# Performance work log

Measured on AMD Instinct MI355X. Metric: run time of the kernel, lower is better.

The kernel has to match this reference:

```python
import jax, jax.numpy as jnp
import numpy as np

NUM_GRAPHS = 256


def _gcn_norm(edge_index, num_nodes):
    # Add self-loops (PyG GCNConv default) and compute symmetric normalization
    loops = jnp.arange(num_nodes, dtype=edge_index.dtype)
    src = jnp.concatenate([edge_index[0], loops])
    dst = jnp.concatenate([edge_index[1], loops])
    deg = jax.ops.segment_sum(jnp.ones_like(dst, dtype=jnp.float32), dst,
                              num_segments=num_nodes)
    dinv = jnp.where(deg > 0, jax.lax.rsqrt(deg), 0.0)
    norm = dinv[src] * dinv[dst]  # [E + N]
    return src, dst, norm


def _gcn_layer(x, W, b, src, dst, norm, num_nodes):
    h = x @ W                      # transform first (cheaper: N x d_out)
    msg = h[src] * norm[:, None]   # gather + per-edge scale  [E+N, d_out]
    agg = jax.ops.segment_sum(msg, dst, num_segments=num_nodes)
    return agg + b


def setup_inputs() -> dict:
    key = jax.random.key(0)
    ks = jax.random.split(key, 12)
    N, E, F_in = 100000, 1600000, 5
    x = jax.random.normal(ks[0], (N, F_in), dtype=jnp.float32)
    edge_index = jax.random.randint(ks[1], (2, E), 0, N, dtype=jnp.int64)
    batch = jnp.sort(jax.random.randint(ks[2], (N,), 0, NUM_GRAPHS, dtype=jnp.int64))

    def glorot(k, fi, fo):
        s = jnp.sqrt(6.0 / (fi + fo))
        return jax.random.uniform(k, (fi, fo), jnp.float32, -s, s)

    return {
        "x": x, "edge_index": edge_index, "batch": batch,
        "W1": glorot(ks[3], F_in, 64), "b1": jnp.zeros((64,), jnp.float32),
        "W2": glorot(ks[4], 64, 128),  "b2": jnp.zeros((128,), jnp.float32),
        "W3": glorot(ks[5], 128, 64),  "b3": jnp.zeros((64,), jnp.float32),
        "Wfc": glorot(ks[6], 64, 1),   "bfc": jnp.zeros((1,), jnp.float32),
    }


def reference(x, edge_index, batch, W1, b1, W2, b2, W3, b3, Wfc, bfc):
    N = x.shape[0]
    src, dst, norm = _gcn_norm(edge_index, N)
    h = jax.nn.relu(_gcn_layer(x, W1, b1, src, dst, norm, N))
    h = jax.nn.relu(_gcn_layer(h, W2, b2, src, dst, norm, N))
    h = jax.nn.relu(_gcn_layer(h, W3, b3, src, dst, norm, N))
    # global mean pool over graph ids
    sums = jax.ops.segment_sum(h, batch, num_segments=NUM_GRAPHS)
    cnts = jax.ops.segment_sum(jnp.ones((N,), jnp.float32), batch,
                               num_segments=NUM_GRAPHS)
    pooled = sums / jnp.maximum(cnts, 1.0)[:, None]   # [G, 64]
    return jax.nn.sigmoid(pooled @ Wfc + bfc)         # [G, 1]
```

## Files before the change

kernel.cpp:

```cpp
#include <hip/hip_runtime.h>
#include <math.h>

#define NG 256
#define NBK 512
#define BCAP 3584
#define FBN 96

static __device__ __forceinline__ int bucket_lo(int p, int n) {
    return (int)(((long long)p * n + NBK - 1) / NBK);
}

static __device__ __forceinline__ float blo(unsigned u) {
    return __uint_as_float(u << 16);
}
static __device__ __forceinline__ float bhi(unsigned u) {
    return __uint_as_float(u & 0xFFFF0000u);
}
static __device__ __forceinline__ unsigned packbf(float a, float b) {
    unsigned ua = __float_as_uint(a);
    ua = (ua + 0x7FFFu + ((ua >> 16) & 1u)) >> 16;
    unsigned ub = __float_as_uint(b);
    ub = (ub + 0x7FFFu + ((ub >> 16) & 1u)) & 0xFFFF0000u;
    return ua | ub;
}

__global__ void zero_bcur(int* bcur) {
    int i = blockIdx.x * blockDim.x + threadIdx.x;
    if (i < NBK) bcur[i] = i * BCAP;
}

__global__ void bucketA(const int* __restrict__ src, const int* __restrict__ dst,
                        int* bcur, unsigned* stage, int e, int n) {
    __shared__ int cnt[NBK];
    __shared__ int base[NBK];
    int nb = gridDim.x;
    int c0 = (int)((long long)blockIdx.x * e / nb);
    int c1 = (int)((long long)(blockIdx.x + 1) * e / nb);
    for (int k = threadIdx.x; k < NBK; k += blockDim.x) cnt[k] = 0;
    __syncthreads();
    for (int i = c0 + threadIdx.x; i < c1; i += blockDim.x) {
        int d = dst[i];
        int p = (int)((long long)d * NBK / n);
        atomicAdd(&cnt[p], 1);
    }
    __syncthreads();
    for (int k = threadIdx.x; k < NBK; k += blockDim.x)
        base[k] = atomicAdd(&bcur[k], cnt[k]);
    __syncthreads();
    for (int k = threadIdx.x; k < NBK; k += blockDim.x) cnt[k] = 0;
    __syncthreads();
    for (int i = c0 + threadIdx.x; i < c1; i += blockDim.x) {
        int s = src[i], d = dst[i];
        int p = (int)((long long)d * NBK / n);
        int ldst = d - bucket_lo(p, n);
        int lp = atomicAdd(&cnt[p], 1);
        stage[base[p] + lp] = ((unsigned)s << 8) | (unsigned)ldst;
    }
}

__global__ void fillB2(const unsigned* __restrict__ stage,
                       const int* __restrict__ bcur,
                       int* __restrict__ rowptr, float* __restrict__ dinv,
                       int* __restrict__ csrs,
                       const float* __restrict__ x, float* __restrict__ xs,
                       int n, int e) {
    __shared__ int ldeg[256];
    __shared__ int loff[256];
    __shared__ int bstart;
    int p = blockIdx.x;
    int t = threadIdx.x;
    int lo = bucket_lo(p, n), hi = bucket_lo(p + 1, n);
    int nloc = hi - lo;

    {
        int acc = 0;
        for (int k = t; k < p; k += 256) acc += bcur[k] - k * BCAP;
        ldeg[t] = acc;
        __syncthreads();
        for (int off = 128; off > 0; off >>= 1) {
            if (t < off) ldeg[t] += ldeg[t + off];
            __syncthreads();
        }
        if (t == 0) bstart = ldeg[0];
        __syncthreads();
    }

    if (t < 256) ldeg[t] = 0;
    __syncthreads();
    int s0 = p * BCAP, s1 = bcur[p];
    for (int i = s0 + t; i < s1; i += 256)
        atomicAdd(&ldeg[stage[i] & 255u], 1);
    __syncthreads();

    int v = (t < nloc) ? ldeg[t] : 0;
    loff[t] = v;
    __syncthreads();
    for (int off = 1; off < 256; off <<= 1) {
        int u = (t >= off) ? loff[t - off] : 0;
        __syncthreads();
        loff[t] += u;
        __syncthreads();
    }
    if (t < nloc) {
        int start = bstart + loff[t] - v;
        rowptr[lo + t] = start;
        float dv = rsqrtf((float)v + 1.0f);
        dinv[lo + t] = dv;
        const float* xr = x + (size_t)(lo + t) * 5;
        float* xo = xs + (size_t)(lo + t) * 5;
#pragma unroll
        for (int k = 0; k < 5; ++k) xo[k] = xr[k] * dv;
    }
    if (p == NBK - 1 && t == 0) rowptr[n] = e;
    __syncthreads();
    if (t < nloc) ldeg[t] = bstart + loff[t] - v;
    __syncthreads();

    for (int i = s0 + t; i < s1; i += 256) {
        unsigned pk = stage[i];
        int ldst = (int)(pk & 255u);
        int pos = atomicAdd(&ldeg[ldst], 1);
        csrs[pos] = (int)(pk >> 8);
    }
}

__global__ void gather5(const int* __restrict__ rowptr,
                        const int* __restrict__ csrs,
                        const float* __restrict__ dinv,
                        const float* __restrict__ xs,
                        float* __restrict__ z, int n) {
    int i = blockIdx.x * blockDim.x + threadIdx.x;
    if (i >= n) return;
    const float* xr = xs + (size_t)i * 5;
    float4 x4 = *(const float4*)(xr);
    float a0 = x4.x, a1 = x4.y, a2 = x4.z, a3 = x4.w, a4 = xr[4];
    int j = rowptr[i], end = rowptr[i + 1], e1 = end - 1;
    for (; j < end; j += 4) {
        int s[4]; float m[4];
#pragma unroll
        for (int k = 0; k < 4; ++k) {
            int jj = j + k;
            s[k] = csrs[jj <= e1 ? jj : e1];
            m[k] = (jj < end) ? 1.0f : 0.0f;
        }
        float4 r4[4]; float r1[4];
#pragma unroll
        for (int k = 0; k < 4; ++k) {
            const float* r = xs + (size_t)s[k] * 5;
            r4[k] = *(const float4*)(r);
            r1[k] = r[4];
        }
#pragma unroll
        for (int k = 0; k < 4; ++k) {
            a0 = fmaf(m[k], r4[k].x, a0);
            a1 = fmaf(m[k], r4[k].y, a1);
            a2 = fmaf(m[k], r4[k].z, a2);
            a3 = fmaf(m[k], r4[k].w, a3);
            a4 = fmaf(m[k], r1[k], a4);
        }
    }
    float di = dinv[i];
    float* zr = z + (size_t)i * 5;
    zr[0] = a0 * di; zr[1] = a1 * di; zr[2] = a2 * di;
    zr[3] = a3 * di; zr[4] = a4 * di;
}

template<int DOUT, bool BR, bool SCALE, bool OUTBF>
static __device__ __forceinline__ void emit(float o[8], const float* b, int c,
                                            float dsc, void* out, int i) {
    if (BR) {
        float4 b0 = *(const float4*)(b + c * 8);
        float4 b1 = *(const float4*)(b + c * 8 + 4);
        o[0] = fmaxf(o[0] + b0.x, 0.f); o[1] = fmaxf(o[1] + b0.y, 0.f);
        o[2] = fmaxf(o[2] + b0.z, 0.f); o[3] = fmaxf(o[3] + b0.w, 0.f);
        o[4] = fmaxf(o[4] + b1.x, 0.f); o[5] = fmaxf(o[5] + b1.y, 0.f);
        o[6] = fmaxf(o[6] + b1.z, 0.f); o[7] = fmaxf(o[7] + b1.w, 0.f);
    }
    if (SCALE) {
#pragma unroll
        for (int q = 0; q < 8; ++q) o[q] *= dsc;
    }
    if (OUTBF) {
        uint4 pk;
        pk.x = packbf(o[0], o[1]); pk.y = packbf(o[2], o[3]);
        pk.z = packbf(o[4], o[5]); pk.w = packbf(o[6], o[7]);
        *(uint4*)((unsigned*)out + (size_t)i * (DOUT / 2) + c * 4) = pk;
    } else {
        float* op = (float*)out + (size_t)i * DOUT + c * 8;
        float4 o0 = {o[0], o[1], o[2], o[3]};
        float4 o1 = {o[4], o[5], o[6], o[7]};
        *(float4*)(op) = o0;
        *(float4*)(op + 4) = o1;
    }
}

template<int DOUT, bool BR, bool SCALE, bool OUTBF, int NODES>
__global__ void transformB5(const float* __restrict__ xin,
                            const float* __restrict__ W,
                            const float* __restrict__ b,
                            const float* __restrict__ dinv,
                            void* __restrict__ out, int n) {
    const int C = DOUT / 8;
    int tid = blockIdx.x * blockDim.x + threadIdx.x;
    int grp = tid / C;
    int c = tid % C;
    int i0 = grp * NODES;
    if (i0 >= n) return;
    float r[NODES][5];
#pragma unroll
    for (int nn = 0; nn < NODES; ++nn) {
        int idx = i0 + nn < n ? i0 + nn : n - 1;
        const float* row = xin + (size_t)idx * 5;
#pragma unroll
        for (int k = 0; k < 5; ++k) r[nn][k] = row[k];
    }
    float acc[NODES][8];
#pragma unroll
    for (int nn = 0; nn < NODES; ++nn)
#pragma unroll
        for (int q = 0; q < 8; ++q) acc[nn][q] = 0.0f;
#pragma unroll
    for (int k = 0; k < 5; ++k) {
        const float* wp = W + (size_t)k * DOUT + c * 8;
        float4 w0 = *(const float4*)(wp);
        float4 w1 = *(const float4*)(wp + 4);
#pragma unroll
        for (int nn = 0; nn < NODES; ++nn) {
            float v = r[nn][k];
            acc[nn][0] = fmaf(v, w0.x, acc[nn][0]);
            acc[nn][1] = fmaf(v, w0.y, acc[nn][1]);
            acc[nn][2] = fmaf(v, w0.z, acc[nn][2]);
            acc[nn][3] = fmaf(v, w0.w, acc[nn][3]);
            acc[nn][4] = fmaf(v, w1.x, acc[nn][4]);
            acc[nn][5] = fmaf(v, w1.y, acc[nn][5]);
            acc[nn][6] = fmaf(v, w1.z, acc[nn][6]);
            acc[nn][7] = fmaf(v, w1.w, acc[nn][7]);
        }
    }
#pragma unroll
    for (int nn = 0; nn < NODES; ++nn) {
        if (i0 + nn >= n) break;
        float dsc = SCALE ? dinv[i0 + nn] : 1.0f;
        emit<DOUT, BR, SCALE, OUTBF>(acc[nn], b, c, dsc, out, i0 + nn);
    }
}

#define ACCA(AA, V) \
    AA[0] += blo(V.x); AA[1] += bhi(V.x); AA[2] += blo(V.y); AA[3] += bhi(V.y); \
    AA[4] += blo(V.z); AA[5] += bhi(V.z); AA[6] += blo(V.w); AA[7] += bhi(V.w);
#define ACCM(AA, V, M) \
    AA[0] = fmaf(M, blo(V.x), AA[0]); AA[1] = fmaf(M, bhi(V.x), AA[1]); \
    AA[2] = fmaf(M, blo(V.y), AA[2]); AA[3] = fmaf(M, bhi(V.y), AA[3]); \
    AA[4] = fmaf(M, blo(V.z), AA[4]); AA[5] = fmaf(M, bhi(V.z), AA[5]); \
    AA[6] = fmaf(M, blo(V.w), AA[6]); AA[7] = fmaf(M, bhi(V.w), AA[7]);

static __device__ __forceinline__ void gather_row(const int* __restrict__ rowptr,
                                                  const int* __restrict__ csrs,
                                                  const unsigned* __restrict__ g,
                                                  int i, int c, float o[8]) {
    uint4 sv = *(const uint4*)(g + (size_t)i * 32 + c * 4);
    float a0[8], a1[8], a2[8], a3[8];
    a0[0] = blo(sv.x); a0[1] = bhi(sv.x); a0[2] = blo(sv.y); a0[3] = bhi(sv.y);
    a0[4] = blo(sv.z); a0[5] = bhi(sv.z); a0[6] = blo(sv.w); a0[7] = bhi(sv.w);
#pragma unroll
    for (int q = 0; q < 8; ++q) { a1[q] = 0.0f; a2[q] = 0.0f; a3[q] = 0.0f; }
    int j = rowptr[i], end = rowptr[i + 1];
    for (; j + 8 <= end; j += 8) {
        uint4 v0 = *(const uint4*)(g + (size_t)csrs[j]     * 32 + c * 4);
        uint4 v1 = *(const uint4*)(g + (size_t)csrs[j + 1] * 32 + c * 4);
        uint4 v2 = *(const uint4*)(g + (size_t)csrs[j + 2] * 32 + c * 4);
        uint4 v3 = *(const uint4*)(g + (size_t)csrs[j + 3] * 32 + c * 4);
        uint4 v4 = *(const uint4*)(g + (size_t)csrs[j + 4] * 32 + c * 4);
        uint4 v5 = *(const uint4*)(g + (size_t)csrs[j + 5] * 32 + c * 4);
        uint4 v6 = *(const uint4*)(g + (size_t)csrs[j + 6] * 32 + c * 4);
        uint4 v7 = *(const uint4*)(g + (size_t)csrs[j + 7] * 32 + c * 4);
        ACCA(a0, v0); ACCA(a1, v1); ACCA(a2, v2); ACCA(a3, v3);
        ACCA(a0, v4); ACCA(a1, v5); ACCA(a2, v6); ACCA(a3, v7);
    }
    if (j < end) {
        int e1 = end - 1;
        int sx[8]; float mm[8];
#pragma unroll
        for (int k = 0; k < 8; ++k) {
            int jj = j + k;
            sx[k] = csrs[jj <= e1 ? jj : e1];
            mm[k] = (jj < end) ? 1.0f : 0.0f;
        }
        uint4 v0 = *(const uint4*)(g + (size_t)sx[0] * 32 + c * 4);
        uint4 v1 = *(const uint4*)(g + (size_t)sx[1] * 32 + c * 4);
        uint4 v2 = *(const uint4*)(g + (size_t)sx[2] * 32 + c * 4);
        uint4 v3 = *(const uint4*)(g + (size_t)sx[3] * 32 + c * 4);
        uint4 v4 = *(const uint4*)(g + (size_t)sx[4] * 32 + c * 4);
        uint4 v5 = *(const uint4*)(g + (size_t)sx[5] * 32 + c * 4);
        uint4 v6 = *(const uint4*)(g + (size_t)sx[6] * 32 + c * 4);
        uint4 v7 = *(const uint4*)(g + (size_t)sx[7] * 32 + c * 4);
        ACCM(a0, v0, mm[0]); ACCM(a1, v1, mm[1]);
        ACCM(a2, v2, mm[2]); ACCM(a3, v3, mm[3]);
        ACCM(a0, v4, mm[4]); ACCM(a1, v5, mm[5]);
        ACCM(a2, v6, mm[6]); ACCM(a3, v7, mm[7]);
    }
#pragma unroll
    for (int q = 0; q < 8; ++q) o[q] = (a0[q] + a1[q]) + (a2[q] + a3[q]);
}

template<bool BR>
__global__ void gatherBF(const int* __restrict__ rowptr,
                         const int* __restrict__ csrs,
                         const float* __restrict__ dinv,
                         const float* __restrict__ b,
                         const unsigned* __restrict__ g,
                         float* __restrict__ z, int n) {
    int tid = blockIdx.x * blockDim.x + threadIdx.x;
    int i = tid >> 3;
    int c = tid & 7;
    if (i >= n) return;
    float o[8];
    gather_row(rowptr, csrs, g, i, c, o);
    float di = dinv[i];
#pragma unroll
    for (int q = 0; q < 8; ++q) o[q] *= di;
    if (BR) {
        float4 b0 = *(const float4*)(b + c * 8);
        float4 b1 = *(const float4*)(b + c * 8 + 4);
        o[0] = fmaxf(o[0] + b0.x, 0.f); o[1] = fmaxf(o[1] + b0.y, 0.f);
        o[2] = fmaxf(o[2] + b0.z, 0.f); o[3] = fmaxf(o[3] + b0.w, 0.f);
        o[4] = fmaxf(o[4] + b1.x, 0.f); o[5] = fmaxf(o[5] + b1.y, 0.f);
        o[6] = fmaxf(o[6] + b1.z, 0.f); o[7] = fmaxf(o[7] + b1.w, 0.f);
    }
    float* zp = z + (size_t)i * 64 + c * 8;
    float4 z0 = {o[0], o[1], o[2], o[3]};
    float4 z1 = {o[4], o[5], o[6], o[7]};
    *(float4*)(zp) = z0;
    *(float4*)(zp + 4) = z1;
}

__global__ void layer23(const int* __restrict__ rowptr,
                        const int* __restrict__ csrs,
                        const float* __restrict__ dinv,
                        const float* __restrict__ b2v,
                        const unsigned* __restrict__ g,
                        const float* __restrict__ W2,
                        const float* __restrict__ W3,
                        unsigned* __restrict__ t3, int n) {
    __shared__ float    z2s[FBN][68];
    __shared__ unsigned h2s[FBN][68];
    int t = threadIdx.x;
    int base = blockIdx.x * FBN;

    {
        int nd = t >> 3, c = t & 7;
        for (int pass = 0; pass < 3; ++pass) {
            int lr = pass * 32 + nd;
            int i = base + lr;
            if (i < n) {
                float o[8];
                gather_row(rowptr, csrs, g, i, c, o);
                float di = dinv[i];
                float4 z0 = {o[0] * di, o[1] * di, o[2] * di, o[3] * di};
                float4 z1 = {o[4] * di, o[5] * di, o[6] * di, o[7] * di};
                *(float4*)&z2s[lr][c * 8] = z0;
                *(float4*)&z2s[lr][c * 8 + 4] = z1;
            }
        }
    }
    __syncthreads();

    {
        int c2 = t & 15;
        int ng = t >> 4;
        float acc[6][8];
#pragma unroll
        for (int nn = 0; nn < 6; ++nn)
#pragma unroll
            for (int q = 0; q < 8; ++q) acc[nn][q] = 0.0f;
        for (int k0 = 0; k0 < 64; k0 += 4) {
            float4 r[6];
#pragma unroll
            for (int nn = 0; nn < 6; ++nn)
                r[nn] = *(const float4*)&z2s[ng + 16 * nn][k0];
#pragma unroll
            for (int kk = 0; kk < 4; ++kk) {
                const float* wp = W2 + (size_t)(k0 + kk) * 128 + c2 * 8;
                float4 w0 = *(const float4*)(wp);
                float4 w1 = *(const float4*)(wp + 4);
#pragma unroll
                for (int nn = 0; nn < 6; ++nn) {
                    float v = (&r[nn].x)[kk];
                    acc[nn][0] = fmaf(v, w0.x, acc[nn][0]);
                    acc[nn][1] = fmaf(v, w0.y, acc[nn][1]);
                    acc[nn][2] = fmaf(v, w0.z, acc[nn][2]);
                    acc[nn][3] = fmaf(v, w0.w, acc[nn][3]);
                    acc[nn][4] = fmaf(v, w1.x, acc[nn][4]);
                    acc[nn][5] = fmaf(v, w1.y, acc[nn][5]);
                    acc[nn][6] = fmaf(v, w1.z, acc[nn][6]);
                    acc[nn][7] = fmaf(v, w1.w, acc[nn][7]);
                }
            }
        }
        float4 b0 = *(const float4*)(b2v + c2 * 8);
        float4 b1 = *(const float4*)(b2v + c2 * 8 + 4);
#pragma unroll
        for (int nn = 0; nn < 6; ++nn) {
            float o[8];
            o[0] = fmaxf(acc[nn][0] + b0.x, 0.f);
            o[1] = fmaxf(acc[nn][1] + b0.y, 0.f);
            o[2] = fmaxf(acc[nn][2] + b0.z, 0.f);
            o[3] = fmaxf(acc[nn][3] + b0.w, 0.f);
            o[4] = fmaxf(acc[nn][4] + b1.x, 0.f);
            o[5] = fmaxf(acc[nn][5] + b1.y, 0.f);
            o[6] = fmaxf(acc[nn][6] + b1.z, 0.f);
            o[7] = fmaxf(acc[nn][7] + b1.w, 0.f);
            uint4 pk;
            pk.x = packbf(o[0], o[1]); pk.y = packbf(o[2], o[3]);
            pk.z = packbf(o[4], o[5]); pk.w = packbf(o[6], o[7]);
            *(uint4*)&h2s[ng + 16 * nn][c2 * 4] = pk;
        }
    }
    __syncthreads();

    {
        int c3 = t & 7;
        int ng = t >> 3;
        float acc[3][8];
#pragma unroll
        for (int nn = 0; nn < 3; ++nn)
#pragma unroll
            for (int q = 0; q < 8; ++q) acc[nn][q] = 0.0f;
        for (int k0 = 0; k0 < 128; k0 += 8) {
            uint4 r[3];
#pragma unroll
            for (int nn = 0; nn < 3; ++nn)
                r[nn] = *(const uint4*)&h2s[ng + 32 * nn][k0 >> 1];
#pragma unroll
            for (int kk = 0; kk < 8; ++kk) {
                const float* wp = W3 + (size_t)(k0 + kk) * 64 + c3 * 8;
                float4 w0 = *(const float4*)(wp);
                float4 w1 = *(const float4*)(wp + 4);
#pragma unroll
                for (int nn = 0; nn < 3; ++nn) {
                    unsigned u = (&r[nn].x)[kk >> 1];
                    float v = (kk & 1) ? bhi(u) : blo(u);
                    acc[nn][0] = fmaf(v, w0.x, acc[nn][0]);
                    acc[nn][1] = fmaf(v, w0.y, acc[nn][1]);
                    acc[nn][2] = fmaf(v, w0.z, acc[nn][2]);
                    acc[nn][3] = fmaf(v, w0.w, acc[nn][3]);
                    acc[nn][4] = fmaf(v, w1.x, acc[nn][4]);
                    acc[nn][5] = fmaf(v, w1.y, acc[nn][5]);
                    acc[nn][6] = fmaf(v, w1.z, acc[nn][6]);
                    acc[nn][7] = fmaf(v, w1.w, acc[nn][7]);
                }
            }
        }
#pragma unroll
        for (int nn = 0; nn < 3; ++nn) {
            int i = base + ng + 32 * nn;
            if (i < n) {
                float ds = dinv[i];
                uint4 pk;
                pk.x = packbf(acc[nn][0] * ds, acc[nn][1] * ds);
                pk.y = packbf(acc[nn][2] * ds, acc[nn][3] * ds);
                pk.z = packbf(acc[nn][4] * ds, acc[nn][5] * ds);
                pk.w = packbf(acc[nn][6] * ds, acc[nn][7] * ds);
                *(uint4*)(t3 + (size_t)i * 32 + c3 * 4) = pk;
            }
        }
    }
}

__global__ void pool(const float* __restrict__ h3, const int* __restrict__ batch,
                     const float* __restrict__ Wfc, const float* __restrict__ bfc,
                     float* __restrict__ out, int n) {
    int g = blockIdx.x;
    int lane = threadIdx.x & 63;
    int w = threadIdx.x >> 6;
    int lo = 0, hi = n;
    while (lo < hi) { int m = (lo + hi) >> 1; if (batch[m] < g) lo = m + 1; else hi = m; }
    int start = lo;
    hi = n;
    while (lo < hi) { int m = (lo + hi) >> 1; if (batch[m] < g + 1) lo = m + 1; else hi = m; }
    int end = lo;
    float a0 = 0.f, a1 = 0.f, a2 = 0.f, a3 = 0.f;
    int m = start + w;
    for (; m + 12 < end; m += 16) {
        a0 += h3[(size_t)m * 64 + lane];
        a1 += h3[(size_t)(m + 4) * 64 + lane];
        a2 += h3[(size_t)(m + 8) * 64 + lane];
        a3 += h3[(size_t)(m + 12) * 64 + lane];
    }
    for (; m < end; m += 4) a0 += h3[(size_t)m * 64 + lane];
    __shared__ float sh[4][64];
    sh[w][lane] = (a0 + a1) + (a2 + a3);
    __syncthreads();
    if (w == 0) {
        float v = (sh[0][lane] + sh[1][lane]) + (sh[2][lane] + sh[3][lane]);
        float cnt = (float)(end - start);
        v = (v / fmaxf(cnt, 1.0f)) * Wfc[lane];
#pragma unroll
        for (int off = 32; off > 0; off >>= 1) v += __shfl_down(v, off, 64);
        if (lane == 0) out[g] = 1.0f / (1.0f + expf(-(v + bfc[0])));
    }
}

static inline int cdiv(long long a, int b) { return (int)((a + b - 1) / b); }

extern "C" void kernel_launch(void* const* d_in, const int* in_sizes, int n_in,
                              void* d_out, int out_size, void* d_ws, size_t ws_size,
                              hipStream_t stream) {
    const float* x   = (const float*)d_in[0];
    const int*   ei  = (const int*)d_in[1];
    const int*   bat = (const int*)d_in[2];
    const float* W1  = (const float*)d_in[3];
    const float* b1  = (const float*)d_in[4];
    const float* W2  = (const float*)d_in[5];
    const float* b2  = (const float*)d_in[6];
    const float* W3  = (const float*)d_in[7];
    const float* b3  = (const float*)d_in[8];
    const float* Wfc = (const float*)d_in[9];
    const float* bfc = (const float*)d_in[10];
    float* out = (float*)d_out;

    const int N = in_sizes[0] / 5;
    const int E = in_sizes[1] / 2;
    const int* src = ei;
    const int* ds  = ei + E;

    char* wsb = (char*)d_ws;
    size_t off = 0;
#define A256(X) (((X) + (size_t)255) & ~(size_t)255)
    float* dinv   = (float*)(wsb + off); off = A256(off + (size_t)N * 4);
    int*   rowptr = (int*)(wsb + off);   off = A256(off + (size_t)(N + 4) * 4);
    int*   bcur   = (int*)(wsb + off);   off = A256(off + (size_t)NBK * 4);
    int*   csrs   = (int*)(wsb + off);   off = A256(off + (size_t)E * 4);
    float* A      = (float*)(wsb + off); off = A256(off + (size_t)N * 128 * 4);
    float* B      = (float*)(wsb + off);
#undef A256
    unsigned* stage = (unsigned*)A;
    float*    xs    = A + (size_t)(1 << 21);
    float*    z1    = A;
    unsigned* h1bf  = (unsigned*)B;
    unsigned* t3bf  = (unsigned*)A;
    float*    h3    = B;

    const int Blk = 256;

    zero_bcur<<<2, 256, 0, stream>>>(bcur);
    bucketA<<<256, 256, 0, stream>>>(src, ds, bcur, stage, E, N);
    fillB2<<<NBK, 256, 0, stream>>>(stage, bcur, rowptr, dinv, csrs, x, xs, N, E);

    gather5<<<cdiv(N, Blk), Blk, 0, stream>>>(rowptr, csrs, dinv, xs, z1, N);
    transformB5<64, true, true, true, 2>
        <<<cdiv((long long)cdiv(N, 2) * 8, Blk), Blk, 0, stream>>>(
        z1, W1, b1, dinv, h1bf, N);

    layer23<<<cdiv(N, FBN), 256, 0, stream>>>(
        rowptr, csrs, dinv, b2, h1bf, W2, W3, t3bf, N);

    gatherBF<true><<<cdiv((long long)N * 8, Blk), Blk, 0, stream>>>(
        rowptr, csrs, dinv, b3, t3bf, h3, N);

    pool<<<NG, 256, 0, stream>>>(h3, bat, Wfc, bfc, out, N);
}
```

Measured before the change: 280.0 us.

## Fuse final GCN gather with mean pooling via global atomics

The last-layer gather now applies bias and ReLU and adds each node's features directly into a per-graph accumulator with global atomicAdd. This removes the intermediate h3 buffer write and its reread by the pooling kernel. A small finish kernel divides by the counts and applies the FC and sigmoid. The risk is heavy atomic contention, since sorted batch ids send many threads to the same 64 addresses, and the summation order becomes nondeterministic.

```diff
diff --git a/kernel.cpp b/kernel.cpp
--- a/kernel.cpp
+++ b/kernel.cpp
@@ -27,6 +27,11 @@
 __global__ void zero_bcur(int* bcur) {
     int i = blockIdx.x * blockDim.x + threadIdx.x;
     if (i < NBK) bcur[i] = i * BCAP;
+}
+
+__global__ void zero_accum(float* accum) {
+    int i = blockIdx.x * blockDim.x + threadIdx.x;
+    if (i < NG * 64) accum[i] = 0.0f;
 }
 
 __global__ void bucketA(const int* __restrict__ src, const int* __restrict__ dst,
@@ -303,13 +308,14 @@
     for (int q = 0; q < 8; ++q) o[q] = (a0[q] + a1[q]) + (a2[q] + a3[q]);
 }
 
-template<bool BR>
-__global__ void gatherBF(const int* __restrict__ rowptr,
-                         const int* __restrict__ csrs,
-                         const float* __restrict__ dinv,
-                         const float* __restrict__ b,
-                         const unsigned* __restrict__ g,
-                         float* __restrict__ z, int n) {
+__global__ void gatherPool(const int* __restrict__ rowptr,
+                           const int* __restrict__ csrs,
+                           const float* __restrict__ dinv,
+                           const float* __restrict__ b,
+                           const unsigned* __restrict__ g,
+                           const int* __restrict__ batch,
+                           float* __restrict__ accum,
+                           int n) {
     int tid = blockIdx.x * blockDim.x + threadIdx.x;
     int i = tid >> 3;
     int c = tid & 7;
@@ -317,21 +323,15 @@
     float o[8];
     gather_row(rowptr, csrs, g, i, c, o);
     float di = dinv[i];
-#pragma unroll
-    for (int q = 0; q < 8; ++q) o[q] *= di;
-    if (BR) {
-        float4 b0 = *(const float4*)(b + c * 8);
-        float4 b1 = *(const float4*)(b + c * 8 + 4);
-        o[0] = fmaxf(o[0] + b0.x, 0.f); o[1] = fmaxf(o[1] + b0.y, 0.f);
-        o[2] = fmaxf(o[2] + b0.z, 0.f); o[3] = fmaxf(o[3] + b0.w, 0.f);
-        o[4] = fmaxf(o[4] + b1.x, 0.f); o[5] = fmaxf(o[5] + b1.y, 0.f);
-        o[6] = fmaxf(o[6] + b1.z, 0.f); o[7] = fmaxf(o[7] + b1.w, 0.f);
-    }
-    float* zp = z + (size_t)i * 64 + c * 8;
-    float4 z0 = {o[0], o[1], o[2], o[3]};
-    float4 z1 = {o[4], o[5], o[6], o[7]};
-    *(float4*)(zp) = z0;
-    *(float4*)(zp + 4) = z1;
+    float4 b0 = *(const float4*)(b + c * 8);
+    float4 b1 = *(const float4*)(b + c * 8 + 4);
+    o[0] = fmaxf(o[0] * di + b0.x, 0.f); o[1] = fmaxf(o[1] * di + b0.y, 0.f);
+    o[2] = fmaxf(o[2] * di + b0.z, 0.f); o[3] = fmaxf(o[3] * di + b0.w, 0.f);
+    o[4] = fmaxf(o[4] * di + b1.x, 0.f); o[5] = fmaxf(o[5] * di + b1.y, 0.f);
+    o[6] = fmaxf(o[6] * di + b1.z, 0.f); o[7] = fmaxf(o[7] * di + b1.w, 0.f);
+    float* ap = accum + (size_t)batch[i] * 64 + c * 8;
+#pragma unroll
+    for (int q = 0; q < 8; ++q) atomicAdd(ap + q, o[q]);
 }
 
 __global__ void layer23(const int* __restrict__ rowptr,
@@ -467,38 +467,24 @@
     }
 }
 
-__global__ void pool(const float* __restrict__ h3, const int* __restrict__ batch,
-                     const float* __restrict__ Wfc, const float* __restrict__ bfc,
-                     float* __restrict__ out, int n) {
+__global__ void finishG(const float* __restrict__ accum,
+                        const int* __restrict__ batch,
+                        const float* __restrict__ Wfc,
+                        const float* __restrict__ bfc,
+                        float* __restrict__ out, int n) {
     int g = blockIdx.x;
-    int lane = threadIdx.x & 63;
-    int w = threadIdx.x >> 6;
+    int lane = threadIdx.x;
     int lo = 0, hi = n;
     while (lo < hi) { int m = (lo + hi) >> 1; if (batch[m] < g) lo = m + 1; else hi = m; }
     int start = lo;
     hi = n;
     while (lo < hi) { int m = (lo + hi) >> 1; if (batch[m] < g + 1) lo = m + 1; else hi = m; }
     int end = lo;
-    float a0 = 0.f, a1 = 0.f, a2 = 0.f, a3 = 0.f;
-    int m = start + w;
-    for (; m + 12 < end; m += 16) {
-        a0 += h3[(size_t)m * 64 + lane];
-        a1 += h3[(size_t)(m + 4) * 64 + lane];
-        a2 += h3[(size_t)(m + 8) * 64 + lane];
-        a3 += h3[(size_t)(m + 12) * 64 + lane];
-    }
-    for (; m < end; m += 4) a0 += h3[(size_t)m * 64 + lane];
-    __shared__ float sh[4][64];
-    sh[w][lane] = (a0 + a1) + (a2 + a3);
-    __syncthreads();
-    if (w == 0) {
-        float v = (sh[0][lane] + sh[1][lane]) + (sh[2][lane] + sh[3][lane]);
-        float cnt = (float)(end - start);
-        v = (v / fmaxf(cnt, 1.0f)) * Wfc[lane];
-#pragma unroll
-        for (int off = 32; off > 0; off >>= 1) v += __shfl_down(v, off, 64);
-        if (lane == 0) out[g] = 1.0f / (1.0f + expf(-(v + bfc[0])));
-    }
+    float cnt = (float)(end - start);
+    float v = (accum[(size_t)g * 64 + lane] / fmaxf(cnt, 1.0f)) * Wfc[lane];
+#pragma unroll
+    for (int off = 32; off > 0; off >>= 1) v += __shfl_down(v, off, 64);
+    if (lane == 0) out[g] = 1.0f / (1.0f + expf(-(v + bfc[0])));
 }
 
 static inline int cdiv(long long a, int b) { return (int)((a + b - 1) / b); }
@@ -530,6 +516,7 @@
     float* dinv   = (float*)(wsb + off); off = A256(off + (size_t)N * 4);
     int*   rowptr = (int*)(wsb + off);   off = A256(off + (size_t)(N + 4) * 4);
     int*   bcur   = (int*)(wsb + off);   off = A256(off + (size_t)NBK * 4);
+    float* accum  = (float*)(wsb + off); off = A256(off + (size_t)NG * 64 * 4);
     int*   csrs   = (int*)(wsb + off);   off = A256(off + (size_t)E * 4);
     float* A      = (float*)(wsb + off); off = A256(off + (size_t)N * 128 * 4);
     float* B      = (float*)(wsb + off);
@@ -539,11 +526,11 @@
     float*    z1    = A;
     unsigned* h1bf  = (unsigned*)B;
     unsigned* t3bf  = (unsigned*)A;
-    float*    h3    = B;
 
     const int Blk = 256;
 
     zero_bcur<<<2, 256, 0, stream>>>(bcur);
+    zero_accum<<<cdiv(NG * 64, 256), 256, 0, stream>>>(accum);
     bucketA<<<256, 256, 0, stream>>>(src, ds, bcur, stage, E, N);
     fillB2<<<NBK, 256, 0, stream>>>(stage, bcur, rowptr, dinv, csrs, x, xs, N, E);
 
@@ -555,8 +542,8 @@
     layer23<<<cdiv(N, FBN), 256, 0, stream>>>(
         rowptr, csrs, dinv, b2, h1bf, W2, W3, t3bf, N);
 
-    gatherBF<true><<<cdiv((long long)N * 8, Blk), Blk, 0, stream>>>(
-        rowptr, csrs, dinv, b3, t3bf, h3, N);
-
-    pool<<<NG, 256, 0, stream>>>(h3, bat, Wfc, bfc, out, N);
-}
+    gatherPool<<<cdiv((long long)N * 8, Blk), Blk, 0, stream>>>(
+        rowptr, csrs, dinv, b3, t3bf, bat, accum, N);
+
+    finishG<<<NG, 64, 0, stream>>>(accum, bat, Wfc, bfc, out, N);
+}
```

Result: slower. 698.3 us (+149.4%).
